# Kernel tuning notes

Measured on AMD Instinct MI355X. Metric: run time of the kernel, lower is better.

## Reference

```python
import jax, jax.numpy as jnp
import numpy as np


def setup_inputs() -> dict:
    key = jax.random.key(0)
    k1, k2 = jax.random.split(key)
    L, B, H = 1024, 64, 1024
    encoder_outputs = jax.random.normal(k1, (L, B, H), dtype=jnp.float32)
    decoder_gru_out = jax.random.normal(k2, (1, B, H), dtype=jnp.float32)
    return {"encoder_outputs": encoder_outputs, "decoder_gru_out": decoder_gru_out}


def reference(encoder_outputs, decoder_gru_out):
    # scores[l,b] = sum_h enc[l,b,h] * dec[0,b,h]
    scores = jnp.einsum('lbh,bh->lb', encoder_outputs, decoder_gru_out[0])
    # softmax over the sequence (L) axis
    attn = jax.nn.softmax(scores, axis=0)  # [L, B]
    # context[b,h] = sum_l attn[l,b] * enc[l,b,h]
    context = jnp.einsum('lb,lbh->bh', attn, encoder_outputs)
    return context
```

## Files before the change

kernel.cpp:

```cpp
#include <hip/hip_runtime.h>
#include <math.h>

#define L_SEQ 1024
#define BATCH 64
#define HDIM  1024
#define WPB   4

#define LOG2E 1.44269504088896340736f

template <int SPLIT, int CHUNK>
__global__ __launch_bounds__(256) void attn_partial_kernel(
    const float* __restrict__ enc, const float* __restrict__ dec,
    float* __restrict__ wsC, float* __restrict__ wsML)
{
    const int tid  = threadIdx.x;
    const int lane = tid & 63;
    const int wave = tid >> 6;
    const int w    = blockIdx.x * WPB + wave;
    const int b    = w / SPLIT;
    const int k    = w - b * SPLIT;
    const int l0   = k * CHUNK;

    const float4* decv = (const float4*)(dec + (size_t)b * HDIM);
    float4 d[4];
    #pragma unroll
    for (int q = 0; q < 4; ++q) d[q] = decv[lane + 64 * q];

    float m = -INFINITY;
    float lsum = 0.0f;
    float4 a[4];
    #pragma unroll
    for (int q = 0; q < 4; ++q) a[q] = make_float4(0.f, 0.f, 0.f, 0.f);

    const size_t row_stride = (size_t)BATCH * HDIM;
    const float* base0 = enc + ((size_t)l0 * BATCH + b) * HDIM;

    float4 B0[4], B1[4];
    auto process = [&](const float4* e) {
        float p = 0.0f;
        #pragma unroll
        for (int q = 0; q < 4; ++q) {
            p = fmaf(e[q].x, d[q].x, p);
            p = fmaf(e[q].y, d[q].y, p);
            p = fmaf(e[q].z, d[q].z, p);
            p = fmaf(e[q].w, d[q].w, p);
        }
        #pragma unroll
        for (int off = 32; off > 0; off >>= 1)
            p += __shfl_xor(p, off, 64);

        const float s = p * LOG2E;
        if (s > m) {
            const float scale = exp2f(m - s);
            lsum *= scale;
            #pragma unroll
            for (int q = 0; q < 4; ++q) {
                a[q].x *= scale;  a[q].y *= scale;
                a[q].z *= scale;  a[q].w *= scale;
            }
            m = s;
        }
        const float wgt = exp2f(s - m);
        lsum += wgt;
        #pragma unroll
        for (int q = 0; q < 4; ++q) {
            a[q].x = fmaf(wgt, e[q].x, a[q].x);
            a[q].y = fmaf(wgt, e[q].y, a[q].y);
            a[q].z = fmaf(wgt, e[q].z, a[q].z);
            a[q].w = fmaf(wgt, e[q].w, a[q].w);
        }
    };

    {
        const float4* row = (const float4*)base0;
        #pragma unroll
        for (int q = 0; q < 4; ++q) B0[q] = row[lane + 64 * q];
    }

    #pragma unroll
    for (int g = 0; g < CHUNK; g += 2) {
        {
            const float4* row = (const float4*)(base0 + (size_t)(g + 1) * row_stride);
            #pragma unroll
            for (int q = 0; q < 4; ++q) B1[q] = row[lane + 64 * q];
        }
        process(B0);
        if (g + 2 < CHUNK) {
            const float4* row = (const float4*)(base0 + (size_t)(g + 2) * row_stride);
            #pragma unroll
            for (int q = 0; q < 4; ++q) B0[q] = row[lane + 64 * q];
        }
        process(B1);
    }

    const size_t r = (size_t)b * SPLIT + k;
    float4* C = (float4*)(wsC + r * (size_t)HDIM);
    #pragma unroll
    for (int q = 0; q < 4; ++q) C[lane + 64 * q] = a[q];
    if (lane == 0) {
        wsML[2 * r]     = m;
        wsML[2 * r + 1] = lsum;
    }
}

__global__ __launch_bounds__(256) void attn_reduce_kernel(
    const float* __restrict__ wsC, const float* __restrict__ wsML,
    float* __restrict__ out, int split)
{
    const int b = blockIdx.x >> 2;
    const int q = blockIdx.x & 3;
    const int h = q * 256 + threadIdx.x;

    float M = -INFINITY;
    for (int k = 0; k < split; ++k)
        M = fmaxf(M, wsML[2 * ((size_t)b * split + k)]);

    float Ltot = 0.0f;
    float acc = 0.0f;
    for (int k = 0; k < split; ++k) {
        const size_t r = (size_t)b * split + k;
        const float wgt = exp2f(wsML[2 * r] - M);
        Ltot = fmaf(wsML[2 * r + 1], wgt, Ltot);
        acc = fmaf(wsC[r * (size_t)HDIM + h], wgt, acc);
    }
    out[(size_t)b * HDIM + h] = acc / Ltot;
}

extern "C" void kernel_launch(void* const* d_in, const int* in_sizes, int n_in,
                              void* d_out, int out_size, void* d_ws, size_t ws_size,
                              hipStream_t stream) {
    const float* enc = (const float*)d_in[0];
    const float* dec = (const float*)d_in[1];
    float* out = (float*)d_out;

    const size_t need64 = (size_t)BATCH * 64 * HDIM * sizeof(float)
                        + (size_t)BATCH * 64 * 2 * sizeof(float);
    float* wsC = (float*)d_ws;

    if (ws_size >= need64) {
        constexpr int SPLIT = 64, CHUNK = L_SEQ / 64;
        float* wsML = wsC + (size_t)BATCH * SPLIT * HDIM;
        attn_partial_kernel<SPLIT, CHUNK>
            <<<(BATCH * SPLIT) / WPB, 256, 0, stream>>>(enc, dec, wsC, wsML);
        attn_reduce_kernel<<<BATCH * 4, 256, 0, stream>>>(wsC, wsML, out, SPLIT);
    } else {
        constexpr int SPLIT = 8, CHUNK = L_SEQ / 8;
        float* wsML = wsC + (size_t)BATCH * SPLIT * HDIM;
        attn_partial_kernel<SPLIT, CHUNK>
            <<<(BATCH * SPLIT) / WPB, 256, 0, stream>>>(enc, dec, wsC, wsML);
        attn_reduce_kernel<<<BATCH * 4, 256, 0, stream>>>(wsC, wsML, out, SPLIT);
    }
}
```

Measured before the change: 379.3 us.

## Double split count and parallelize reduce across waves with float4 loads

Result: faster. 370.4 us (-2.3%).

```diff
diff --git a/kernel.cpp b/kernel.cpp
--- a/kernel.cpp
+++ b/kernel.cpp
@@ -103,27 +103,64 @@
     }
 }
 
+template <int SPLIT>
 __global__ __launch_bounds__(256) void attn_reduce_kernel(
     const float* __restrict__ wsC, const float* __restrict__ wsML,
-    float* __restrict__ out, int split)
+    float* __restrict__ out)
 {
-    const int b = blockIdx.x >> 2;
-    const int q = blockIdx.x & 3;
-    const int h = q * 256 + threadIdx.x;
+    constexpr int KPW = SPLIT / 4;
+    const int b  = blockIdx.x >> 2;
+    const int hq = blockIdx.x & 3;
+    const int wv = threadIdx.x >> 6;
+    const int ln = threadIdx.x & 63;
+    const int h4 = hq * 64 + ln;
 
-    float M = -INFINITY;
-    for (int k = 0; k < split; ++k)
-        M = fmaxf(M, wsML[2 * ((size_t)b * split + k)]);
+    float mw = -INFINITY;
+    #pragma unroll 4
+    for (int i = 0; i < KPW; ++i) {
+        const int r = b * SPLIT + wv + 4 * i;
+        mw = fmaxf(mw, wsML[2 * r]);
+    }
 
-    float Ltot = 0.0f;
-    float acc = 0.0f;
-    for (int k = 0; k < split; ++k) {
-        const size_t r = (size_t)b * split + k;
-        const float wgt = exp2f(wsML[2 * r] - M);
-        Ltot = fmaf(wsML[2 * r + 1], wgt, Ltot);
-        acc = fmaf(wsC[r * (size_t)HDIM + h], wgt, acc);
+    float lt = 0.0f;
+    float4 acc = make_float4(0.f, 0.f, 0.f, 0.f);
+    #pragma unroll 4
+    for (int i = 0; i < KPW; ++i) {
+        const int r = b * SPLIT + wv + 4 * i;
+        const float wgt = exp2f(wsML[2 * r] - mw);
+        lt = fmaf(wsML[2 * r + 1], wgt, lt);
+        const float4 c = ((const float4*)(wsC + (size_t)r * HDIM))[h4];
+        acc.x = fmaf(wgt, c.x, acc.x);
+        acc.y = fmaf(wgt, c.y, acc.y);
+        acc.z = fmaf(wgt, c.z, acc.z);
+        acc.w = fmaf(wgt, c.w, acc.w);
     }
-    out[(size_t)b * HDIM + h] = acc / Ltot;
+
+    __shared__ float4 lacc[4][64];
+    __shared__ float  lml[4][2];
+    lacc[wv][ln] = acc;
+    if (ln == 0) { lml[wv][0] = mw; lml[wv][1] = lt; }
+    __syncthreads();
+
+    if (wv == 0) {
+        const float M = fmaxf(fmaxf(lml[0][0], lml[1][0]),
+                              fmaxf(lml[2][0], lml[3][0]));
+        const float w0 = exp2f(lml[0][0] - M);
+        const float w1 = exp2f(lml[1][0] - M);
+        const float w2 = exp2f(lml[2][0] - M);
+        const float w3 = exp2f(lml[3][0] - M);
+        const float Lt = lml[0][1] * w0 + lml[1][1] * w1
+                       + lml[2][1] * w2 + lml[3][1] * w3;
+        const float inv = 1.0f / Lt;
+        const float4 a0 = lacc[0][ln], a1 = lacc[1][ln];
+        const float4 a2 = lacc[2][ln], a3 = lacc[3][ln];
+        float4 o;
+        o.x = (a0.x * w0 + a1.x * w1 + a2.x * w2 + a3.x * w3) * inv;
+        o.y = (a0.y * w0 + a1.y * w1 + a2.y * w2 + a3.y * w3) * inv;
+        o.z = (a0.z * w0 + a1.z * w1 + a2.z * w2 + a3.z * w3) * inv;
+        o.w = (a0.w * w0 + a1.w * w1 + a2.w * w2 + a3.w * w3) * inv;
+        ((float4*)(out + (size_t)b * HDIM))[h4] = o;
+    }
 }
 
 extern "C" void kernel_launch(void* const* d_in, const int* in_sizes, int n_in,
@@ -133,21 +170,21 @@
     const float* dec = (const float*)d_in[1];
     float* out = (float*)d_out;
 
-    const size_t need64 = (size_t)BATCH * 64 * HDIM * sizeof(float)
-                        + (size_t)BATCH * 64 * 2 * sizeof(float);
+    const size_t need128 = (size_t)BATCH * 128 * HDIM * sizeof(float)
+                         + (size_t)BATCH * 128 * 2 * sizeof(float);
     float* wsC = (float*)d_ws;
 
-    if (ws_size >= need64) {
-        constexpr int SPLIT = 64, CHUNK = L_SEQ / 64;
+    if (ws_size >= need128) {
+        constexpr int SPLIT = 128, CHUNK = L_SEQ / 128;
         float* wsML = wsC + (size_t)BATCH * SPLIT * HDIM;
         attn_partial_kernel<SPLIT, CHUNK>
             <<<(BATCH * SPLIT) / WPB, 256, 0, stream>>>(enc, dec, wsC, wsML);
-        attn_reduce_kernel<<<BATCH * 4, 256, 0, stream>>>(wsC, wsML, out, SPLIT);
+        attn_reduce_kernel<SPLIT><<<BATCH * 4, 256, 0, stream>>>(wsC, wsML, out);
     } else {
         constexpr int SPLIT = 8, CHUNK = L_SEQ / 8;
         float* wsML = wsC + (size_t)BATCH * SPLIT * HDIM;
         attn_partial_kernel<SPLIT, CHUNK>
             <<<(BATCH * SPLIT) / WPB, 256, 0, stream>>>(enc, dec, wsC, wsML);
-        attn_reduce_kernel<<<BATCH * 4, 256, 0, stream>>>(wsC, wsML, out, SPLIT);
+        attn_reduce_kernel<SPLIT><<<BATCH * 4, 256, 0, stream>>>(wsC, wsML, out);
     }
 }
```

## Fuse split-L reduction into partial kernel via last-block atomic counter

Applied to the files above, without the earlier changes.

New measurement: 485.4 us. +28.0%, slower.

```diff
diff --git a/kernel.cpp b/kernel.cpp
--- a/kernel.cpp
+++ b/kernel.cpp
@@ -9,10 +9,12 @@
 #define LOG2E 1.44269504088896340736f
 
 template <int SPLIT, int CHUNK>
-__global__ __launch_bounds__(256) void attn_partial_kernel(
+__global__ __launch_bounds__(256) void attn_fused_kernel(
     const float* __restrict__ enc, const float* __restrict__ dec,
-    float* __restrict__ wsC, float* __restrict__ wsML)
+    float* __restrict__ wsC, float* __restrict__ wsML,
+    unsigned int* __restrict__ cnt, float* __restrict__ out)
 {
+    constexpr int BPB = SPLIT / WPB;
     const int tid  = threadIdx.x;
     const int lane = tid & 63;
     const int wave = tid >> 6;
@@ -76,7 +78,6 @@
         #pragma unroll
         for (int q = 0; q < 4; ++q) B0[q] = row[lane + 64 * q];
     }
-
     #pragma unroll
     for (int g = 0; g < CHUNK; g += 2) {
         {
@@ -101,29 +102,42 @@
         wsML[2 * r]     = m;
         wsML[2 * r + 1] = lsum;
     }
-}
 
-__global__ __launch_bounds__(256) void attn_reduce_kernel(
-    const float* __restrict__ wsC, const float* __restrict__ wsML,
-    float* __restrict__ out, int split)
-{
-    const int b = blockIdx.x >> 2;
-    const int q = blockIdx.x & 3;
-    const int h = q * 256 + threadIdx.x;
+    __syncthreads();
+    __shared__ unsigned int s_old;
+    if (tid == 0) {
+        __threadfence();
+        s_old = atomicAdd(&cnt[b], 1u);
+    }
+    __syncthreads();
+    if (s_old != BPB - 1) return;
 
+    __threadfence();
+
+    const float* mlb = wsML + 2 * (size_t)b * SPLIT;
     float M = -INFINITY;
-    for (int k = 0; k < split; ++k)
-        M = fmaxf(M, wsML[2 * ((size_t)b * split + k)]);
+    #pragma unroll 8
+    for (int kk = 0; kk < SPLIT; ++kk)
+        M = fmaxf(M, mlb[2 * kk]);
 
-    float Ltot = 0.0f;
-    float acc = 0.0f;
-    for (int k = 0; k < split; ++k) {
-        const size_t r = (size_t)b * split + k;
-        const float wgt = exp2f(wsML[2 * r] - M);
-        Ltot = fmaf(wsML[2 * r + 1], wgt, Ltot);
-        acc = fmaf(wsC[r * (size_t)HDIM + h], wgt, acc);
+    float Lt = 0.0f;
+    float4 acc = make_float4(0.f, 0.f, 0.f, 0.f);
+    const float4* Cb = (const float4*)(wsC + (size_t)b * SPLIT * HDIM);
+    #pragma unroll 4
+    for (int kk = 0; kk < SPLIT; ++kk) {
+        const float wgt = exp2f(mlb[2 * kk] - M);
+        Lt = fmaf(mlb[2 * kk + 1], wgt, Lt);
+        const float4 c = Cb[(size_t)kk * (HDIM / 4) + tid];
+        acc.x = fmaf(wgt, c.x, acc.x);
+        acc.y = fmaf(wgt, c.y, acc.y);
+        acc.z = fmaf(wgt, c.z, acc.z);
+        acc.w = fmaf(wgt, c.w, acc.w);
     }
-    out[(size_t)b * HDIM + h] = acc / Ltot;
+    const float inv = 1.0f / Lt;
+    float4 o;
+    o.x = acc.x * inv;  o.y = acc.y * inv;
+    o.z = acc.z * inv;  o.w = acc.w * inv;
+    ((float4*)(out + (size_t)b * HDIM))[tid] = o;
 }
 
 extern "C" void kernel_launch(void* const* d_in, const int* in_sizes, int n_in,
@@ -133,21 +147,25 @@
     const float* dec = (const float*)d_in[1];
     float* out = (float*)d_out;
 
-    const size_t need64 = (size_t)BATCH * 64 * HDIM * sizeof(float)
-                        + (size_t)BATCH * 64 * 2 * sizeof(float);
+    constexpr int SPLIT = 64, CHUNK = L_SEQ / SPLIT;
+    const size_t need = (size_t)BATCH * SPLIT * HDIM * sizeof(float)
+                      + (size_t)BATCH * SPLIT * 2 * sizeof(float)
+                      + (size_t)BATCH * sizeof(unsigned int);
+
     float* wsC = (float*)d_ws;
+    float* wsML = wsC + (size_t)BATCH * SPLIT * HDIM;
+    unsigned int* cnt = (unsigned int*)(wsML + 2 * (size_t)BATCH * SPLIT);
 
-    if (ws_size >= need64) {
-        constexpr int SPLIT = 64, CHUNK = L_SEQ / 64;
-        float* wsML = wsC + (size_t)BATCH * SPLIT * HDIM;
-        attn_partial_kernel<SPLIT, CHUNK>
-            <<<(BATCH * SPLIT) / WPB, 256, 0, stream>>>(enc, dec, wsC, wsML);
-        attn_reduce_kernel<<<BATCH * 4, 256, 0, stream>>>(wsC, wsML, out, SPLIT);
+    if (ws_size >= need) {
+        hipMemsetAsync(cnt, 0, BATCH * sizeof(unsigned int), stream);
+        attn_fused_kernel<SPLIT, CHUNK>
+            <<<(BATCH * SPLIT) / WPB, 256, 0, stream>>>(enc, dec, wsC, wsML, cnt, out);
     } else {
-        constexpr int SPLIT = 8, CHUNK = L_SEQ / 8;
-        float* wsML = wsC + (size_t)BATCH * SPLIT * HDIM;
-        attn_partial_kernel<SPLIT, CHUNK>
-            <<<(BATCH * SPLIT) / WPB, 256, 0, stream>>>(enc, dec, wsC, wsML);
-        attn_reduce_kernel<<<BATCH * 4, 256, 0, stream>>>(wsC, wsML, out, SPLIT);
+        constexpr int S2 = 8, C2 = L_SEQ / S2;
+        float* wsML2 = wsC + (size_t)BATCH * S2 * HDIM;
+        unsigned int* cnt2 = (unsigned int*)(wsML2 + 2 * (size_t)BATCH * S2);
+        hipMemsetAsync(cnt2, 0, BATCH * sizeof(unsigned int), stream);
+        attn_fused_kernel<S2, C2>
+            <<<(BATCH * S2) / WPB, 256, 0, stream>>>(enc, dec, wsC, wsML2, cnt2, out);
     }
 }
```
